# Kernel tuning notes

Measured on AMD Instinct MI355X. Metric: run time of the kernel, lower is better.

## Reference

```python
import jax, jax.numpy as jnp
import numpy as np

B, S, D, H, M = 4, 2048, 1024, 16, 128
DH = D // H
SCALE = jnp.float32(np.sqrt(D / H))


def setup_inputs() -> dict:
    key = jax.random.key(0)
    ks = jax.random.split(key, 4)
    x = jax.random.normal(ks[0], (B, S, D), dtype=jnp.float32)
    mask = jnp.zeros((B, 1, 1, S), dtype=bool)
    W_in = jax.random.normal(ks[1], (3 * D, D), dtype=jnp.float32) * 0.02
    b_in = jnp.zeros((3 * D,), dtype=jnp.float32)
    pos_emb = jax.random.normal(ks[2], (2 * M + 1, DH), dtype=jnp.float32)
    W_out = jax.random.normal(ks[3], (D, D), dtype=jnp.float32) * 0.02
    b_out = jnp.zeros((D,), dtype=jnp.float32)
    return {"x": x, "mask": mask, "W_in": W_in, "b_in": b_in,
            "pos_emb": pos_emb, "W_out": W_out, "b_out": b_out}


def _arrange_pos(pos_emb, seq_len, max_len):
    k = jnp.arange(seq_len)
    q = jnp.arange(seq_len)
    idx = jnp.clip(k[None, :] - q[:, None], -max_len, max_len) + max_len  # [S,S]
    return pos_emb[idx]  # [S,S,DH]


def reference(x, mask, W_in, b_in, pos_emb, W_out, b_out):
    b, s, d = x.shape
    qkv = x @ W_in.T + b_in                      # [B,S,3D]
    qkv = qkv.reshape(b, s, H, 3 * DH).transpose(0, 2, 1, 3)  # [B,H,S,3DH]
    Q, K, V = jnp.split(qkv, 3, axis=3)          # each [B,H,S,DH]
    logits = jnp.einsum('bhqd,bhkd->bhqk', Q, K)
    rel = _arrange_pos(pos_emb, s, M)            # [S,S,DH] (q,k,dh)
    pos_logits = jnp.einsum('bhqd,qkd->bhqk', Q, rel)
    logits = (logits + pos_logits) / SCALE
    logits = jnp.where(mask, -jnp.inf, logits)
    attn = jax.nn.softmax(logits, axis=3)
    combined = jnp.einsum('bhqk,bhkd->bhqd', attn, V)
    out = combined.transpose(0, 2, 1, 3).reshape(b, s, d)  # concat heads
    return out @ W_out.T + b_out
```

## Files before the change

kernel.cpp:

```cpp
#include <hip/hip_runtime.h>
#include <hip/hip_bf16.h>
#include <math.h>

#define SS 2048
#define HH 16
#define NPOS 257
#define C_SCALE 0.18033688f
#define DTHR 8.0f

typedef short  s16x8 __attribute__((ext_vector_type(8)));
typedef float  f32x4 __attribute__((ext_vector_type(4)));
typedef unsigned u32x4 __attribute__((ext_vector_type(4)));

__device__ __forceinline__ unsigned short f2bf(float f) {
    unsigned u = __builtin_bit_cast(unsigned, f);
    u += 0x7fff + ((u >> 16) & 1);
    return (unsigned short)(u >> 16);
}
__device__ __forceinline__ float bf2f(unsigned short b) {
    return __builtin_bit_cast(float, (unsigned)b << 16);
}
__device__ __forceinline__ s16x8 pack8(float4 a, float4 b) {
    s16x8 v;
    v[0]=(short)f2bf(a.x); v[1]=(short)f2bf(a.y); v[2]=(short)f2bf(a.z); v[3]=(short)f2bf(a.w);
    v[4]=(short)f2bf(b.x); v[5]=(short)f2bf(b.y); v[6]=(short)f2bf(b.z); v[7]=(short)f2bf(b.w);
    return v;
}
__device__ __forceinline__ unsigned cvtpk(float lo, float hi) {
    unsigned r;
    asm("v_cvt_pk_bf16_f32 %0, %1, %2" : "=v"(r) : "v"(lo), "v"(hi));
    return r;
}
__device__ __forceinline__ float exp2_fast(float x) {
    float r;
    asm("v_exp_f32 %0, %1" : "=v"(r) : "v"(x));
    return r;
}
__device__ __forceinline__ f32x4 mfma16(s16x8 a, s16x8 b, f32x4 c) {
    return __builtin_amdgcn_mfma_f32_16x16x32_bf16(a, b, c, 0, 0, 0);
}
__device__ __forceinline__ void gload_lds16(const void* gsrc, void* ldst) {
    __builtin_amdgcn_global_load_lds(
        (const __attribute__((address_space(1))) unsigned int*)gsrc,
        (__attribute__((address_space(3))) unsigned int*)ldst,
        16, 0, 0);
}
__device__ __forceinline__ int colp(int k) {
    return ((k >> 5) << 6) | (((k >> 2) & 3) << 4) | (((k >> 4) & 1) << 3) | ((k & 3) << 1);
}

__global__ __launch_bounds__(256)
void cvt_bf16(const float* __restrict__ in, unsigned short* __restrict__ out, int n8)
{
    for (int i = blockIdx.x * blockDim.x + threadIdx.x; i < n8; i += gridDim.x * blockDim.x) {
        const float4* p = (const float4*)(in + (size_t)i * 8);
        *(s16x8*)(out + (size_t)i * 8) = pack8(p[0], p[1]);
    }
}

__global__ __launch_bounds__(256)
void gemm_bf16_nt(const unsigned short* __restrict__ A,
                  const unsigned short* __restrict__ Bm,
                  const float* __restrict__ bias, float* __restrict__ Cout,
                  int Ndim, int Kdim)
{
    __shared__ short As[128 * 32];
    __shared__ short Bs[128 * 32];
    const int tid  = threadIdx.x;
    const int lane = tid & 63;
    const int wv   = tid >> 6;
    const int g    = lane >> 4;
    const int ln   = lane & 15;
    const int wm   = wv >> 1, wn = wv & 1;
    const int tm   = blockIdx.y << 7, tn = blockIdx.x << 7;
    const int srow  = lane >> 2;
    const int sslot = lane & 3;

    f32x4 acc[4][4];
#pragma unroll
    for (int mi = 0; mi < 4; ++mi)
#pragma unroll
        for (int ni = 0; ni < 4; ++ni) acc[mi][ni] = f32x4{0.f, 0.f, 0.f, 0.f};

    const unsigned short* Ab = A  + (size_t)(tm + wv*32 + srow) * Kdim + sslot*8;
    const unsigned short* Bb = Bm + (size_t)(tn + wv*32 + srow) * Kdim + sslot*8;
    const size_t rstep16 = (size_t)16 * Kdim;
    char* lA = (char*)As + (wv*32) * 64;
    char* lB = (char*)Bs + (wv*32) * 64;

    for (int k0 = 0; k0 < Kdim; k0 += 32) {
        __syncthreads();
        gload_lds16(Ab + k0,           lA);
        gload_lds16(Ab + k0 + rstep16, lA + 1024);
        gload_lds16(Bb + k0,           lB);
        gload_lds16(Bb + k0 + rstep16, lB + 1024);
        __syncthreads();

        s16x8 af[4], bf_[4];
#pragma unroll
        for (int mi = 0; mi < 4; ++mi)
            af[mi] = *(const s16x8*)((char*)As + (wm*64 + mi*16 + ln)*64 + g*16);
#pragma unroll
        for (int ni = 0; ni < 4; ++ni)
            bf_[ni] = *(const s16x8*)((char*)Bs + (wn*64 + ni*16 + ln)*64 + g*16);
#pragma unroll
        for (int mi = 0; mi < 4; ++mi)
#pragma unroll
            for (int ni = 0; ni < 4; ++ni)
                acc[mi][ni] = mfma16(af[mi], bf_[ni], acc[mi][ni]);
    }

#pragma unroll
    for (int ni = 0; ni < 4; ++ni) {
        const int col = tn + wn*64 + ni*16 + ln;
        const float bcol = bias[col];
#pragma unroll
        for (int mi = 0; mi < 4; ++mi)
#pragma unroll
            for (int j = 0; j < 4; ++j) {
                const int row = tm + wm*64 + mi*16 + 4*g + j;
                Cout[(size_t)row * Ndim + col] = acc[mi][ni][j] + bcol;
            }
    }
}

__global__ __launch_bounds__(256)
void gemm_qkv(const unsigned short* __restrict__ A,
              const unsigned short* __restrict__ Bm,
              const float* __restrict__ bias,
              unsigned short* __restrict__ qb,
              char* __restrict__ kbuf, char* __restrict__ vbuf)
{
    __shared__ short As[128 * 32];
    __shared__ short Bs[128 * 32];
    const int tid  = threadIdx.x;
    const int lane = tid & 63;
    const int wv   = tid >> 6;
    const int g    = lane >> 4;
    const int ln   = lane & 15;
    const int wm   = wv >> 1, wn = wv & 1;
    const int tm   = blockIdx.y << 7, tn = blockIdx.x << 7;
    const int srow  = lane >> 2;
    const int sslot = lane & 3;
    const int Kdim = 1024;

    f32x4 acc[4][4];
#pragma unroll
    for (int mi = 0; mi < 4; ++mi)
#pragma unroll
        for (int ni = 0; ni < 4; ++ni) acc[mi][ni] = f32x4{0.f, 0.f, 0.f, 0.f};

    const unsigned short* Ab = A  + (size_t)(tm + wv*32 + srow) * Kdim + sslot*8;
    const unsigned short* Bb = Bm + (size_t)(tn + wv*32 + srow) * Kdim + sslot*8;
    const size_t rstep16 = (size_t)16 * Kdim;
    char* lA = (char*)As + (wv*32) * 64;
    char* lB = (char*)Bs + (wv*32) * 64;

    for (int k0 = 0; k0 < Kdim; k0 += 32) {
        __syncthreads();
        gload_lds16(Ab + k0,           lA);
        gload_lds16(Ab + k0 + rstep16, lA + 1024);
        gload_lds16(Bb + k0,           lB);
        gload_lds16(Bb + k0 + rstep16, lB + 1024);
        __syncthreads();

        s16x8 af[4], bf_[4];
#pragma unroll
        for (int mi = 0; mi < 4; ++mi)
            af[mi] = *(const s16x8*)((char*)As + (wm*64 + mi*16 + ln)*64 + g*16);
#pragma unroll
        for (int ni = 0; ni < 4; ++ni)
            bf_[ni] = *(const s16x8*)((char*)Bs + (wn*64 + ni*16 + ln)*64 + g*16);
#pragma unroll
        for (int mi = 0; mi < 4; ++mi)
#pragma unroll
            for (int ni = 0; ni < 4; ++ni)
                acc[mi][ni] = mfma16(af[mi], bf_[ni], acc[mi][ni]);
    }

#pragma unroll
    for (int ni = 0; ni < 4; ++ni) {
        const int col  = tn + wn*64 + ni*16 + ln;
        const int col0 = tn + wn*64 + ni*16;
        const int h    = col0 / 192;
        const int r0   = col0 - h*192;
        const int r    = r0 + ln;
        const float bcol = bias[col];
#pragma unroll
        for (int mi = 0; mi < 4; ++mi) {
            const int rowb = tm + wm*64 + mi*16 + 4*g;
            const int bb = rowb >> 11, sl = rowb & 2047;
            const int kt = sl >> 6, kr = sl & 63;
            const size_t tile = ((size_t)(bb*HH + h)*32 + kt) * 8192;
            if (r0 < 64) {
                unsigned short* qp = qb + (((size_t)(bb*HH + h))*SS + sl)*64 + r;
#pragma unroll
                for (int j = 0; j < 4; ++j)
                    qp[(size_t)j*64] = f2bf(acc[mi][ni][j] + bcol);
            } else if (r0 < 128) {
                const int d = r - 64;
#pragma unroll
                for (int j = 0; j < 4; ++j) {
                    const int krj = kr + j;
                    *(unsigned short*)(kbuf + tile + krj*128 + ((2*d) ^ ((krj&7)<<4))) =
                        f2bf(acc[mi][ni][j] + bcol);
                }
            } else {
                const int d = r - 128;
                uint2 w;
                w.x = cvtpk(acc[mi][ni][0] + bcol, acc[mi][ni][1] + bcol);
                w.y = cvtpk(acc[mi][ni][2] + bcol, acc[mi][ni][3] + bcol);
                *(uint2*)(vbuf + tile + d*128 + (colp(kr) ^ ((d&7)<<4))) = w;
            }
        }
    }
}

#define FAR_LDS  32768
#define NEAR_LDS (32768 + 64*260*2)

__global__ __launch_bounds__(128, 2)
void attn_far(const unsigned short* __restrict__ qb,
              const char* __restrict__ kbuf, const char* __restrict__ vbuf,
              const unsigned short* __restrict__ pos_bf,
              float* __restrict__ o_state,
              float* __restrict__ m_state,
              float* __restrict__ l_state)
{
    extern __shared__ char smem[];
    char* ksb = smem;
    char* vtb = smem + 16384;

    const int tid = threadIdx.x, lane = tid & 63, wv = tid >> 6;
    const int g = lane >> 4, ln = lane & 15;
    const int fid = ((blockIdx.x & 7) << 7) | (blockIdx.x >> 3);
    const int q0 = (fid & 15) << 7, h = (fid >> 4) & 15, b = fid >> 8;
    const int q0w = q0 + wv*64;
    const int swz = (ln & 7) << 4;

    const unsigned short* qhb = qb + ((size_t)(b*HH + h))*SS*64;
    const char* ktile = kbuf + (size_t)(b*HH + h)*32*8192;
    const char* vtile = vbuf + (size_t)(b*HH + h)*32*8192;
    const char* ssrc = wv ? vtile : ktile;
    char*       sdst = wv ? vtb   : ksb;

    s16x8 qf[4][2];
#pragma unroll
    for (int gg = 0; gg < 4; ++gg) {
        const unsigned short* qp = qhb + (size_t)(q0w + 16*gg + ln) * 64;
        qf[gg][0] = *(const s16x8*)(qp + 8*g);
        qf[gg][1] = *(const s16x8*)(qp + 32 + 8*g);
    }

#define F_STAGE(kt, buf) do {                                                 \
        const char* s_ = ssrc + (size_t)(kt)*8192 + lane*16;                  \
        char* d_ = sdst + (buf)*8192;                                         \
        _Pragma("unroll")                                                     \
        for (int i_ = 0; i_ < 8; ++i_)                                        \
            gload_lds16(s_ + i_*1024, d_ + i_*1024);                          \
    } while (0)

    const int ktA = max(0, (q0 - 128) >> 6);
    const int ktB = min(32, (q0 + 256) >> 6);
    const int gap = ktB - ktA, nfar = 32 - gap;

    F_STAGE((0 < ktA) ? 0 : gap, 0);

    float blo[4], bhi[4];
    {
        const int bsrc = (ln >> 2) << 4;
        const int s3 = ln & 3;
#pragma unroll
        for (int pass = 0; pass < 2; ++pass) {
            const int c  = pass*256 + ln;
            const int cc = c > 256 ? 256 : c;
            const unsigned short* pp = pos_bf + (size_t)cc * 64;
            s16x8 b0 = *(const s16x8*)(pp + 8*g);
            s16x8 b1 = *(const s16x8*)(pp + 32 + 8*g);
#pragma unroll
            for (int gg = 0; gg < 4; ++gg) {
                f32x4 d = {0,0,0,0};
                d = mfma16(qf[gg][0], b0, d);
                d = mfma16(qf[gg][1], b1, d);
                const float r0 = __shfl(d[0]*C_SCALE, bsrc, 64);
                const float r1 = __shfl(d[1]*C_SCALE, bsrc, 64);
                const float r2 = __shfl(d[2]*C_SCALE, bsrc, 64);
                const float r3 = __shfl(d[3]*C_SCALE, bsrc, 64);
                const float r = s3 == 0 ? r0 : s3 == 1 ? r1 : s3 == 2 ? r2 : r3;
                if (pass == 0) blo[gg] = r; else bhi[gg] = r;
            }
        }
    }
    __syncthreads();

    f32x4 o[4][4], l[4];
    float m[4];
#pragma unroll
    for (int gg = 0; gg < 4; ++gg) {
        m[gg] = -INFINITY; l[gg] = f32x4{0,0,0,0};
#pragma unroll
        for (int dt = 0; dt < 4; ++dt) o[gg][dt] = f32x4{0,0,0,0};
    }
    s16x8 ONES;
#pragma unroll
    for (int i = 0; i < 8; ++i) ONES[i] = (short)0x3F80;

    for (int v = 0; v < nfar; ++v) {
        const int kt = (v < ktA) ? v : v + gap;
        const char* kbp = ksb + (v & 1)*8192;
        const char* vbp = vtb + (v & 1)*8192;
        if (v + 1 < nfar)
            F_STAGE((v + 1 < ktA) ? v + 1 : v + 1 + gap, (v + 1) & 1);

        u32x4 pa[4][2];
#pragma unroll
        for (int hf = 0; hf < 2; ++hf) {
            f32x4 s[2][4];
#pragma unroll
            for (int gi = 0; gi < 2; ++gi)
#pragma unroll
                for (int t = 0; t < 4; ++t) s[gi][t] = f32x4{0,0,0,0};
            __builtin_amdgcn_s_setprio(1);
#pragma unroll
            for (int kc = 0; kc < 2; ++kc) {
                s16x8 kf[4];
#pragma unroll
                for (int t = 0; t < 4; ++t)
                    kf[t] = *(const s16x8*)(kbp + (t*16 + ln)*128 + ((kc*64 + g*16) ^ swz));
#pragma unroll
                for (int t = 0; t < 4; ++t)
#pragma unroll
                    for (int gi = 0; gi < 2; ++gi)
                        s[gi][t] = mfma16(kf[t], qf[2*hf + gi][kc], s[gi][t]);
            }
            __builtin_amdgcn_s_setprio(0);

            float mx[2];
#pragma unroll
            for (int gi = 0; gi < 2; ++gi) {
                const int gg = 2*hf + gi;
                const float bc = (kt < ktA) ? blo[gg] : bhi[gg];
                float m0 = -INFINITY;
#pragma unroll
                for (int t = 0; t < 4; ++t)
#pragma unroll
                    for (int j = 0; j < 4; ++j) {
                        s[gi][t][j] = s[gi][t][j]*C_SCALE + bc;
                        m0 = fmaxf(m0, s[gi][t][j]);
                    }
                mx[gi] = m0;
            }
            if (__any(fmaxf(mx[0] - m[2*hf], mx[1] - m[2*hf+1]) > DTHR)) {
#pragma unroll
                for (int gi = 0; gi < 2; ++gi) {
                    const int gg = 2*hf + gi;
                    float mr = mx[gi];
                    mr = fmaxf(mr, __shfl_xor(mr, 16, 64));
                    mr = fmaxf(mr, __shfl_xor(mr, 32, 64));
                    const float nm = fmaxf(m[gg], mr);
                    const float corr = exp2_fast(m[gg] - nm);
                    m[gg] = nm;
#pragma unroll
                    for (int j = 0; j < 4; ++j) {
                        const float cj = __shfl(corr, (lane & 48) + 4*g + j, 64);
#pragma unroll
                        for (int dt = 0; dt < 4; ++dt) o[gg][dt][j] *= cj;
                        l[gg][j] *= cj;
                    }
                }
            }
#pragma unroll
            for (int gi = 0; gi < 2; ++gi) {
                const int gg = 2*hf + gi;
#pragma unroll
                for (int t = 0; t < 4; ++t) {
                    const float p0 = exp2_fast(s[gi][t][0] - m[gg]);
                    const float p1 = exp2_fast(s[gi][t][1] - m[gg]);
                    const float p2 = exp2_fast(s[gi][t][2] - m[gg]);
                    const float p3 = exp2_fast(s[gi][t][3] - m[gg]);
                    pa[gg][t>>1][2*(t&1)]   = cvtpk(p0, p1);
                    pa[gg][t>>1][2*(t&1)+1] = cvtpk(p2, p3);
                }
            }
        }

        __builtin_amdgcn_s_setprio(1);
#pragma unroll
        for (int kc = 0; kc < 2; ++kc) {
#pragma unroll
            for (int dt = 0; dt < 4; ++dt) {
                const s16x8 bv = *(const s16x8*)(vbp + (dt*16 + ln)*128 + ((kc*64 + g*16) ^ swz));
#pragma unroll
                for (int gg = 0; gg < 4; ++gg)
                    o[gg][dt] = mfma16(__builtin_bit_cast(s16x8, pa[gg][kc]), bv, o[gg][dt]);
            }
#pragma unroll
            for (int gg = 0; gg < 4; ++gg)
                l[gg] = mfma16(__builtin_bit_cast(s16x8, pa[gg][kc]), ONES, l[gg]);
        }
        __builtin_amdgcn_s_setprio(0);

        __syncthreads();
    }

    const size_t rbase = (((size_t)(b*HH + h)) << 11) + q0w;
#pragma unroll
    for (int gg = 0; gg < 4; ++gg) {
        if (lane < 16) m_state[rbase + 16*gg + ln] = m[gg];
        if (ln == 0) {
#pragma unroll
            for (int j = 0; j < 4; ++j) l_state[rbase + 16*gg + 4*g + j] = l[gg][j];
        }
#pragma unroll
        for (int dt = 0; dt < 4; ++dt)
#pragma unroll
            for (int j = 0; j < 4; ++j)
                o_state[(rbase + 16*gg + 4*g + j)*64 + dt*16 + ln] = o[gg][dt][j];
    }
}

__global__ __launch_bounds__(256, 2)
void attn_near(const unsigned short* __restrict__ qb,
               const char* __restrict__ kbuf, const char* __restrict__ vbuf,
               const unsigned short* __restrict__ pos_bf,
               const float* __restrict__ o_state,
               const float* __restrict__ m_state,
               const float* __restrict__ l_state,
               unsigned short* __restrict__ comb)
{
    extern __shared__ char smem[];
    char* ksb = smem;
    char* vtb = smem + 16384;
    unsigned short* tab = (unsigned short*)(smem + 32768);

    const int tid = threadIdx.x, lane = tid & 63, wv = tid >> 6;
    const int g = lane >> 4, ln = lane & 15;
    const int fid = ((blockIdx.x & 7) << 8) | (blockIdx.x >> 3);
    const int q0 = (fid & 31) << 6, h = (fid >> 5) & 15, b = fid >> 9;
    const int q0w = q0 + wv*16;
    const int swz = (ln & 7) << 4;

    const unsigned short* qhb = qb + ((size_t)(b*HH + h))*SS*64;
    const char* ktile = kbuf + (size_t)(b*HH + h)*32*8192;
    const char* vtile = vbuf + (size_t)(b*HH + h)*32*8192;
    const int sv    = wv >> 1;
    const int shalf = (wv & 1) * 4096;
    const char* ssrc = sv ? vtile : ktile;
    char*       sdst = sv ? vtb   : ksb;

    s16x8 qf[2];
    {
        const unsigned short* qp = qhb + (size_t)(q0w + ln) * 64;
        qf[0] = *(const s16x8*)(qp + 8*g);
        qf[1] = *(const s16x8*)(qp + 32 + 8*g);
    }

#define N_STAGE(kt, buf) do {                                                 \
        const char* s_ = ssrc + (size_t)(kt)*8192 + shalf + lane*16;          \
        char* d_ = sdst + (buf)*8192 + shalf;                                 \
        _Pragma("unroll")                                                     \
        for (int i_ = 0; i_ < 4; ++i_)                                        \
            gload_lds16(s_ + i_*1024, d_ + i_*1024);                          \
    } while (0)

    const int q0p = q0 & ~127;
    const int ktA = max(0, (q0p - 128) >> 6);
    const int ktB = min(32, (q0p + 256) >> 6);
    const int ntile = ktB - ktA;

    N_STAGE(ktA, 0);

    for (int ct = 0; ct < 17; ++ct) {
        const int c  = ct*16 + ln;
        const int cc = c > 256 ? 256 : c;
        const unsigned short* pp = pos_bf + (size_t)cc * 64;
        s16x8 b0 = *(const s16x8*)(pp + 8*g);
        s16x8 b1 = *(const s16x8*)(pp + 32 + 8*g);
        f32x4 d = {0,0,0,0};
        d = mfma16(qf[0], b0, d);
        d = mfma16(qf[1], b1, d);
        if (c < NPOS) {
#pragma unroll
            for (int j = 0; j < 4; ++j)
                tab[(16*wv + 4*g + j)*260 + c] = f2bf(d[j] * C_SCALE);
        }
    }
    __syncthreads();

    const size_t rbase = (((size_t)(b*HH + h)) << 11) + q0w;
    float m_run = m_state[rbase + ln];
    f32x4 l_acc;
#pragma unroll
    for (int j = 0; j < 4; ++j) l_acc[j] = l_state[rbase + 4*g + j];
    f32x4 o_acc[4];
#pragma unroll
    for (int dt = 0; dt < 4; ++dt)
#pragma unroll
        for (int j = 0; j < 4; ++j)
            o_acc[dt][j] = o_state[(rbase + 4*g + j)*64 + dt*16 + ln];

    const int rowb = (16*wv + ln) * 260;
    const int coff = 4*g - 16*wv - ln + 128 - q0;
    s16x8 ONES;
#pragma unroll
    for (int i = 0; i < 8; ++i) ONES[i] = (short)0x3F80;

    for (int v = 0; v < ntile; ++v) {
        const int kt = ktA + v;
        const char* kbp = ksb + (v & 1)*8192;
        const char* vbp = vtb + (v & 1)*8192;
        if (v + 1 < ntile) N_STAGE(kt + 1, (v + 1) & 1);

        f32x4 s[4];
#pragma unroll
        for (int t = 0; t < 4; ++t) s[t] = f32x4{0,0,0,0};
        __builtin_amdgcn_s_setprio(1);
#pragma unroll
        for (int kc = 0; kc < 2; ++kc) {
            s16x8 kf[4];
#pragma unroll
            for (int t = 0; t < 4; ++t)
                kf[t] = *(const s16x8*)(kbp + (t*16 + ln)*128 + ((kc*64 + g*16) ^ swz));
#pragma unroll
            for (int t = 0; t < 4; ++t)
                s[t] = mfma16(kf[t], qf[kc], s[t]);
        }
        __builtin_amdgcn_s_setprio(0);

        const int colb = (kt << 6) + coff;
        float mx = -INFINITY;
#pragma unroll
        for (int t = 0; t < 4; ++t)
#pragma unroll
            for (int j = 0; j < 4; ++j) {
                int c = colb + 16*t + j;
                c = c < 0 ? 0 : (c > 256 ? 256 : c);
                s[t][j] = s[t][j]*C_SCALE + bf2f(tab[rowb + c]);
                mx = fmaxf(mx, s[t][j]);
            }

        if (__any(mx > m_run + DTHR)) {
            float mr = mx;
            mr = fmaxf(mr, __shfl_xor(mr, 16, 64));
            mr = fmaxf(mr, __shfl_xor(mr, 32, 64));
            const float nm = fmaxf(m_run, mr);
            const float corr = exp2_fast(m_run - nm);
            m_run = nm;
#pragma unroll
            for (int j = 0; j < 4; ++j) {
                const float cj = __shfl(corr, (lane & 48) + 4*g + j, 64);
#pragma unroll
                for (int dt = 0; dt < 4; ++dt) o_acc[dt][j] *= cj;
                l_acc[j] *= cj;
            }
        }

        u32x4 pa[2];
#pragma unroll
        for (int t = 0; t < 4; ++t) {
            const float p0 = exp2_fast(s[t][0] - m_run);
            const float p1 = exp2_fast(s[t][1] - m_run);
            const float p2 = exp2_fast(s[t][2] - m_run);
            const float p3 = exp2_fast(s[t][3] - m_run);
            pa[t>>1][2*(t&1)]   = cvtpk(p0, p1);
            pa[t>>1][2*(t&1)+1] = cvtpk(p2, p3);
        }

        __builtin_amdgcn_s_setprio(1);
#pragma unroll
        for (int kc = 0; kc < 2; ++kc) {
            const s16x8 pA_ = __builtin_bit_cast(s16x8, pa[kc]);
#pragma unroll
            for (int dt = 0; dt < 4; ++dt) {
                const s16x8 bv = *(const s16x8*)(vbp + (dt*16 + ln)*128 + ((kc*64 + g*16) ^ swz));
                o_acc[dt] = mfma16(pA_, bv, o_acc[dt]);
            }
            l_acc = mfma16(pA_, ONES, l_acc);
        }
        __builtin_amdgcn_s_setprio(0);

        __syncthreads();
    }

    f32x4 inv;
#pragma unroll
    for (int j = 0; j < 4; ++j) inv[j] = 1.0f / l_acc[j];
#pragma unroll
    for (int dt = 0; dt < 4; ++dt)
#pragma unroll
        for (int j = 0; j < 4; ++j)
            comb[((size_t)b*SS + q0w + 4*g + j)*1024 + h*64 + dt*16 + ln] =
                f2bf(o_acc[dt][j] * inv[j]);
}

extern "C" void kernel_launch(void* const* d_in, const int* in_sizes, int n_in,
                              void* d_out, int out_size, void* d_ws, size_t ws_size,
                              hipStream_t stream)
{
    const float* x     = (const float*)d_in[0];
    const float* W_in  = (const float*)d_in[2];
    const float* b_in  = (const float*)d_in[3];
    const float* pos   = (const float*)d_in[4];
    const float* W_out = (const float*)d_in[5];
    const float* b_out = (const float*)d_in[6];
    float* out = (float*)d_out;

    char* ws = (char*)d_ws;
    unsigned short* q_buf   = (unsigned short*)(ws);
    char*           k_buf   = (char*)          (ws +  16777216);
    char*           v_buf   = (char*)          (ws +  33554432);
    unsigned short* comb_bf = (unsigned short*)(ws +  50331648);
    unsigned short* x_bf    = (unsigned short*)(ws +  67108864);
    unsigned short* wi_bf   = (unsigned short*)(ws +  83886080);
    unsigned short* wo_bf   = (unsigned short*)(ws +  90177536);
    unsigned short* pos_bf  = (unsigned short*)(ws +  92274688);
    float*          o_state = (float*)        (ws +  92340224);
    float*          m_state = (float*)        (ws + 125894656);
    float*          l_state = (float*)        (ws + 126418944);

    cvt_bf16<<<2048, 256, 0, stream>>>(x,     x_bf,  8192*1024/8);
    cvt_bf16<<<1024, 256, 0, stream>>>(W_in,  wi_bf, 3072*1024/8);
    cvt_bf16<<<512,  256, 0, stream>>>(W_out, wo_bf, 1024*1024/8);
    cvt_bf16<<<9,    256, 0, stream>>>(pos,   pos_bf, 2056);

    gemm_qkv<<<dim3(24, 64), 256, 0, stream>>>(x_bf, wi_bf, b_in, q_buf, k_buf, v_buf);

    (void)hipFuncSetAttribute((const void*)attn_far,
                              hipFuncAttributeMaxDynamicSharedMemorySize, FAR_LDS);
    attn_far<<<dim3(1024), 128, FAR_LDS, stream>>>(q_buf, k_buf, v_buf, pos_bf,
                                                   o_state, m_state, l_state);

    (void)hipFuncSetAttribute((const void*)attn_near,
                              hipFuncAttributeMaxDynamicSharedMemorySize, NEAR_LDS);
    attn_near<<<dim3(2048), 256, NEAR_LDS, stream>>>(q_buf, k_buf, v_buf, pos_bf,
                                                     o_state, m_state, l_state, comb_bf);

    gemm_bf16_nt<<<dim3(8, 64), 256, 0, stream>>>(comb_bf, wo_bf, b_out, out, 1024, 1024);
}
```

Baseline: 259.5 us.

## Fold softmax scale into Q, speculate exp before max, load V to registers

The softmax scale is applied to Q when the projection writes it, so the attention kernels no longer multiply logits by it. The online softmax now computes exponentials against the old running max first, and only recomputes them after a max update when any probability exceeds a threshold. This removes the separate max-reduction pass from the common path. In the far kernel V tiles are read straight from global memory into registers, and only K is staged through LDS (halving its shared memory). The cost is more register pressure, exposed global-load latency for V, and the threshold adding some numerical risk.

```diff
diff --git a/kernel.cpp b/kernel.cpp
--- a/kernel.cpp
+++ b/kernel.cpp
@@ -6,7 +6,7 @@
 #define HH 16
 #define NPOS 257
 #define C_SCALE 0.18033688f
-#define DTHR 8.0f
+#define P_THR 256.0f
 
 typedef short  s16x8 __attribute__((ext_vector_type(8)));
 typedef float  f32x4 __attribute__((ext_vector_type(4)));
@@ -196,7 +196,7 @@
                 unsigned short* qp = qb + (((size_t)(bb*HH + h))*SS + sl)*64 + r;
 #pragma unroll
                 for (int j = 0; j < 4; ++j)
-                    qp[(size_t)j*64] = f2bf(acc[mi][ni][j] + bcol);
+                    qp[(size_t)j*64] = f2bf((acc[mi][ni][j] + bcol) * C_SCALE);
             } else if (r0 < 128) {
                 const int d = r - 64;
 #pragma unroll
@@ -216,7 +216,7 @@
     }
 }
 
-#define FAR_LDS  32768
+#define FAR_LDS  16384
 #define NEAR_LDS (32768 + 64*260*2)
 
 __global__ __launch_bounds__(128, 2)
@@ -229,7 +229,6 @@
 {
     extern __shared__ char smem[];
     char* ksb = smem;
-    char* vtb = smem + 16384;
 
     const int tid = threadIdx.x, lane = tid & 63, wv = tid >> 6;
     const int g = lane >> 4, ln = lane & 15;
@@ -241,8 +240,6 @@
     const unsigned short* qhb = qb + ((size_t)(b*HH + h))*SS*64;
     const char* ktile = kbuf + (size_t)(b*HH + h)*32*8192;
     const char* vtile = vbuf + (size_t)(b*HH + h)*32*8192;
-    const char* ssrc = wv ? vtile : ktile;
-    char*       sdst = wv ? vtb   : ksb;
 
     s16x8 qf[4][2];
 #pragma unroll
@@ -252,19 +249,34 @@
         qf[gg][1] = *(const s16x8*)(qp + 32 + 8*g);
     }
 
-#define F_STAGE(kt, buf) do {                                                 \
-        const char* s_ = ssrc + (size_t)(kt)*8192 + lane*16;                  \
-        char* d_ = sdst + (buf)*8192;                                         \
+    s16x8 vf[8];
+
+#define F_STAGE_K(kt, buf) do {                                               \
+        const char* s_ = ktile + (size_t)(kt)*8192 + wv*4096 + lane*16;       \
+        char* d_ = ksb + (buf)*8192 + wv*4096;                                \
         _Pragma("unroll")                                                     \
-        for (int i_ = 0; i_ < 8; ++i_)                                        \
+        for (int i_ = 0; i_ < 4; ++i_)                                        \
             gload_lds16(s_ + i_*1024, d_ + i_*1024);                          \
+    } while (0)
+#define F_LOAD_V(kt) do {                                                     \
+        const char* s_ = vtile + (size_t)(kt)*8192;                           \
+        _Pragma("unroll")                                                     \
+        for (int kc_ = 0; kc_ < 2; ++kc_)                                     \
+            _Pragma("unroll")                                                 \
+            for (int dt_ = 0; dt_ < 4; ++dt_)                                 \
+                vf[kc_*4+dt_] = *(const s16x8*)(s_ + (dt_*16 + ln)*128 +      \
+                                                ((kc_*64 + g*16) ^ swz));     \
     } while (0)
 
     const int ktA = max(0, (q0 - 128) >> 6);
     const int ktB = min(32, (q0 + 256) >> 6);
     const int gap = ktB - ktA, nfar = 32 - gap;
 
-    F_STAGE((0 < ktA) ? 0 : gap, 0);
+    {
+        const int kt0 = (0 < ktA) ? 0 : gap;
+        F_STAGE_K(kt0, 0);
+        F_LOAD_V(kt0);
+    }
 
     float blo[4], bhi[4];
     {
@@ -282,10 +294,10 @@
                 f32x4 d = {0,0,0,0};
                 d = mfma16(qf[gg][0], b0, d);
                 d = mfma16(qf[gg][1], b1, d);
-                const float r0 = __shfl(d[0]*C_SCALE, bsrc, 64);
-                const float r1 = __shfl(d[1]*C_SCALE, bsrc, 64);
-                const float r2 = __shfl(d[2]*C_SCALE, bsrc, 64);
-                const float r3 = __shfl(d[3]*C_SCALE, bsrc, 64);
+                const float r0 = __shfl(d[0], bsrc, 64);
+                const float r1 = __shfl(d[1], bsrc, 64);
+                const float r2 = __shfl(d[2], bsrc, 64);
+                const float r3 = __shfl(d[3], bsrc, 64);
                 const float r = s3 == 0 ? r0 : s3 == 1 ? r1 : s3 == 2 ? r2 : r3;
                 if (pass == 0) blo[gg] = r; else bhi[gg] = r;
             }
@@ -308,9 +320,8 @@
     for (int v = 0; v < nfar; ++v) {
         const int kt = (v < ktA) ? v : v + gap;
         const char* kbp = ksb + (v & 1)*8192;
-        const char* vbp = vtb + (v & 1)*8192;
-        if (v + 1 < nfar)
-            F_STAGE((v + 1 < ktA) ? v + 1 : v + 1 + gap, (v + 1) & 1);
+        const int ktn = (v + 1 < ktA) ? v + 1 : v + 1 + gap;
+        if (v + 1 < nfar) F_STAGE_K(ktn, (v + 1) & 1);
 
         u32x4 pa[4][2];
 #pragma unroll
@@ -335,29 +346,37 @@
             }
             __builtin_amdgcn_s_setprio(0);
 
-            float mx[2];
+            float pmax[2];
 #pragma unroll
             for (int gi = 0; gi < 2; ++gi) {
                 const int gg = 2*hf + gi;
-                const float bc = (kt < ktA) ? blo[gg] : bhi[gg];
-                float m0 = -INFINITY;
-#pragma unroll
-                for (int t = 0; t < 4; ++t)
-#pragma unroll
-                    for (int j = 0; j < 4; ++j) {
-                        s[gi][t][j] = s[gi][t][j]*C_SCALE + bc;
-                        m0 = fmaxf(m0, s[gi][t][j]);
-                    }
-                mx[gi] = m0;
-            }
-            if (__any(fmaxf(mx[0] - m[2*hf], mx[1] - m[2*hf+1]) > DTHR)) {
+                const float bmv = ((kt < ktA) ? blo[gg] : bhi[gg]) - m[gg];
+                float pm = 0.f;
+#pragma unroll
+                for (int t = 0; t < 4; ++t) {
+                    const float p0 = exp2_fast(s[gi][t][0] + bmv);
+                    const float p1 = exp2_fast(s[gi][t][1] + bmv);
+                    const float p2 = exp2_fast(s[gi][t][2] + bmv);
+                    const float p3 = exp2_fast(s[gi][t][3] + bmv);
+                    pm = fmaxf(pm, fmaxf(fmaxf(p0, p1), fmaxf(p2, p3)));
+                    pa[gg][t>>1][2*(t&1)]   = cvtpk(p0, p1);
+                    pa[gg][t>>1][2*(t&1)+1] = cvtpk(p2, p3);
+                }
+                pmax[gi] = pm;
+            }
+            if (__any(fmaxf(pmax[0], pmax[1]) > P_THR)) {
 #pragma unroll
                 for (int gi = 0; gi < 2; ++gi) {
                     const int gg = 2*hf + gi;
-                    float mr = mx[gi];
+                    const float bc = (kt < ktA) ? blo[gg] : bhi[gg];
+                    float mr = s[gi][0][0];
+#pragma unroll
+                    for (int t = 0; t < 4; ++t)
+#pragma unroll
+                        for (int j = 0; j < 4; ++j) mr = fmaxf(mr, s[gi][t][j]);
                     mr = fmaxf(mr, __shfl_xor(mr, 16, 64));
                     mr = fmaxf(mr, __shfl_xor(mr, 32, 64));
-                    const float nm = fmaxf(m[gg], mr);
+                    const float nm = fmaxf(m[gg], mr + bc);
                     const float corr = exp2_fast(m[gg] - nm);
                     m[gg] = nm;
 #pragma unroll
@@ -367,21 +386,18 @@
                         for (int dt = 0; dt < 4; ++dt) o[gg][dt][j] *= cj;
                         l[gg][j] *= cj;
                     }
+                    const float nb = bc - nm;
+#pragma unroll
+                    for (int t = 0; t < 4; ++t) {
+                        const float p0 = exp2_fast(s[gi][t][0] + nb);
+                        const float p1 = exp2_fast(s[gi][t][1] + nb);
+                        const float p2 = exp2_fast(s[gi][t][2] + nb);
+                        const float p3 = exp2_fast(s[gi][t][3] + nb);
+                        pa[gg][t>>1][2*(t&1)]   = cvtpk(p0, p1);
+                        pa[gg][t>>1][2*(t&1)+1] = cvtpk(p2, p3);
+                    }
                 }
             }
-#pragma unroll
-            for (int gi = 0; gi < 2; ++gi) {
-                const int gg = 2*hf + gi;
-#pragma unroll
-                for (int t = 0; t < 4; ++t) {
-                    const float p0 = exp2_fast(s[gi][t][0] - m[gg]);
-                    const float p1 = exp2_fast(s[gi][t][1] - m[gg]);
-                    const float p2 = exp2_fast(s[gi][t][2] - m[gg]);
-                    const float p3 = exp2_fast(s[gi][t][3] - m[gg]);
-                    pa[gg][t>>1][2*(t&1)]   = cvtpk(p0, p1);
-                    pa[gg][t>>1][2*(t&1)+1] = cvtpk(p2, p3);
-                }
-            }
         }
 
         __builtin_amdgcn_s_setprio(1);
@@ -389,7 +405,7 @@
         for (int kc = 0; kc < 2; ++kc) {
 #pragma unroll
             for (int dt = 0; dt < 4; ++dt) {
-                const s16x8 bv = *(const s16x8*)(vbp + (dt*16 + ln)*128 + ((kc*64 + g*16) ^ swz));
+                const s16x8 bv = vf[kc*4 + dt];
 #pragma unroll
                 for (int gg = 0; gg < 4; ++gg)
                     o[gg][dt] = mfma16(__builtin_bit_cast(s16x8, pa[gg][kc]), bv, o[gg][dt]);
@@ -400,6 +416,7 @@
         }
         __builtin_amdgcn_s_setprio(0);
 
+        if (v + 1 < nfar) F_LOAD_V(ktn);
         __syncthreads();
     }
 
@@ -482,7 +499,7 @@
         if (c < NPOS) {
 #pragma unroll
             for (int j = 0; j < 4; ++j)
-                tab[(16*wv + 4*g + j)*260 + c] = f2bf(d[j] * C_SCALE);
+                tab[(16*wv + 4*g + j)*260 + c] = f2bf(d[j]);
         }
     }
     __syncthreads();
@@ -528,19 +545,33 @@
         __builtin_amdgcn_s_setprio(0);
 
         const int colb = (kt << 6) + coff;
-        float mx = -INFINITY;
 #pragma unroll
         for (int t = 0; t < 4; ++t)
 #pragma unroll
             for (int j = 0; j < 4; ++j) {
                 int c = colb + 16*t + j;
                 c = c < 0 ? 0 : (c > 256 ? 256 : c);
-                s[t][j] = s[t][j]*C_SCALE + bf2f(tab[rowb + c]);
-                mx = fmaxf(mx, s[t][j]);
-            }
-
-        if (__any(mx > m_run + DTHR)) {
-            float mr = mx;
+                s[t][j] = s[t][j] + bf2f(tab[rowb + c]);
+            }
+
+        u32x4 pa[2];
+        float pm = 0.f;
+#pragma unroll
+        for (int t = 0; t < 4; ++t) {
+            const float p0 = exp2_fast(s[t][0] - m_run);
+            const float p1 = exp2_fast(s[t][1] - m_run);
+            const float p2 = exp2_fast(s[t][2] - m_run);
+            const float p3 = exp2_fast(s[t][3] - m_run);
+            pm = fmaxf(pm, fmaxf(fmaxf(p0, p1), fmaxf(p2, p3)));
+            pa[t>>1][2*(t&1)]   = cvtpk(p0, p1);
+            pa[t>>1][2*(t&1)+1] = cvtpk(p2, p3);
+        }
+        if (__any(pm > P_THR)) {
+            float mr = s[0][0];
+#pragma unroll
+            for (int t = 0; t < 4; ++t)
+#pragma unroll
+                for (int j = 0; j < 4; ++j) mr = fmaxf(mr, s[t][j]);
             mr = fmaxf(mr, __shfl_xor(mr, 16, 64));
             mr = fmaxf(mr, __shfl_xor(mr, 32, 64));
             const float nm = fmaxf(m_run, mr);
@@ -553,17 +584,15 @@
                 for (int dt = 0; dt < 4; ++dt) o_acc[dt][j] *= cj;
                 l_acc[j] *= cj;
             }
-        }
-
-        u32x4 pa[2];
-#pragma unroll
-        for (int t = 0; t < 4; ++t) {
-            const float p0 = exp2_fast(s[t][0] - m_run);
-            const float p1 = exp2_fast(s[t][1] - m_run);
-            const float p2 = exp2_fast(s[t][2] - m_run);
-            const float p3 = exp2_fast(s[t][3] - m_run);
-            pa[t>>1][2*(t&1)]   = cvtpk(p0, p1);
-            pa[t>>1][2*(t&1)+1] = cvtpk(p2, p3);
+#pragma unroll
+            for (int t = 0; t < 4; ++t) {
+                const float p0 = exp2_fast(s[t][0] - m_run);
+                const float p1 = exp2_fast(s[t][1] - m_run);
+                const float p2 = exp2_fast(s[t][2] - m_run);
+                const float p3 = exp2_fast(s[t][3] - m_run);
+                pa[t>>1][2*(t&1)]   = cvtpk(p0, p1);
+                pa[t>>1][2*(t&1)+1] = cvtpk(p2, p3);
+            }
         }
 
         __builtin_amdgcn_s_setprio(1);
```

New measurement: 256.6 us. About the same (-1.1%).
